# Optimization experiments

Measured on AMD Instinct MI355X. Metric: run time of the kernel, lower is better.

The kernel has to match this reference:

```python
import jax, jax.numpy as jnp
import numpy as np

B, C, H, W = 4, 512, 64, 64
RED = 8
D = max(1, C // RED)  # inter_channels = 64
BN_EPS = 1e-5


def conv1x1(x, w, b):
    # x: [B,Cin,H,W], w: [Cout,Cin], b: [Cout]
    return jnp.einsum('oc,bchw->bohw', w, x) + b[None, :, None, None]


def setup_inputs() -> dict:
    key = jax.random.key(0)
    ks = jax.random.split(key, 12)
    s = 0.02
    return {
        'x': jax.random.normal(ks[0], (B, C, H, W), jnp.float32),
        'theta_w': jax.random.normal(ks[1], (D, C), jnp.float32) * s,
        'theta_b': jax.random.normal(ks[2], (D,), jnp.float32) * s,
        'phi_w': jax.random.normal(ks[3], (D, C), jnp.float32) * s,
        'phi_b': jax.random.normal(ks[4], (D,), jnp.float32) * s,
        'g_w': jax.random.normal(ks[5], (D, C), jnp.float32) * s,
        'g_b': jax.random.normal(ks[6], (D,), jnp.float32) * s,
        'out_w': jax.random.normal(ks[7], (C, D), jnp.float32) * s,
        'out_b': jax.random.normal(ks[8], (C,), jnp.float32) * s,
        'bn_gamma': jnp.ones((C,), jnp.float32),
        'bn_beta': jnp.zeros((C,), jnp.float32),
        'scale': jax.random.normal(ks[9], (1,), jnp.float32) * 0.1,
    }


def reference(x, theta_w, theta_b, phi_w, phi_b, g_w, g_b,
              out_w, out_b, bn_gamma, bn_beta, scale):
    b, c, h, w = x.shape
    n = h * w
    theta = conv1x1(x, theta_w, theta_b).reshape(b, D, n)  # [B,D,N]
    phi = conv1x1(x, phi_w, phi_b).reshape(b, D, n)        # [B,D,N]
    g = conv1x1(x, g_w, g_b).reshape(b, D, n)              # [B,D,N]
    # attention[b,i,j] = sum_d theta[b,d,i] * phi[b,d,j] (unscaled)
    attn = jax.nn.softmax(jnp.einsum('bdi,bdj->bij', theta, phi), axis=-1)
    # y[b,d,i] = sum_j g[b,d,j] * attn[b,i,j]
    y = jnp.einsum('bdj,bij->bdi', g, attn).reshape(b, D, h, w)
    y = conv1x1(y, out_w, out_b)  # [B,C,H,W]
    # BatchNorm2d, training-mode batch statistics over (B,H,W)
    mean = jnp.mean(y, axis=(0, 2, 3), keepdims=True)
    var = jnp.var(y, axis=(0, 2, 3), keepdims=True)
    y = (y - mean) * jax.lax.rsqrt(var + BN_EPS)
    y = y * bn_gamma[None, :, None, None] + bn_beta[None, :, None, None]
    return x + scale.reshape(()) * y
```

## Files before the change

### kernel.cpp

```cpp
#include <hip/hip_runtime.h>
#include <hip/hip_bf16.h>
#include <math.h>

#define NPIX 4096
#define CIN  512
#define DD   64
#define BB   4
#define NCHUNK 8

using f32x4  = __attribute__((ext_vector_type(4))) float;
using bf16x8 = __attribute__((ext_vector_type(8))) short;
using u16x4  = __attribute__((ext_vector_type(4))) unsigned short;

__device__ __forceinline__ unsigned short f2bf(float f){
    union { __hip_bfloat16 h; unsigned short u; } v;
    v.h = __float2bfloat16(f);
    return v.u;
}

__device__ __forceinline__ unsigned pk2(float a, float b){
    union { __hip_bfloat162 h; unsigned u; } v;
    v.h = __float22bfloat162_rn(make_float2(a, b));
    return v.u;
}

__device__ __forceinline__ bf16x8 cvt8(float4 a, float4 b){
    union { unsigned u[4]; bf16x8 v; } r;
    r.u[0] = pk2(a.x, a.y); r.u[1] = pk2(a.z, a.w);
    r.u[2] = pk2(b.x, b.y); r.u[3] = pk2(b.z, b.w);
    return r.v;
}

__global__ __launch_bounds__(256) void k0_xt(
    const float* __restrict__ x, unsigned short* __restrict__ xT)
{
    const int n0 = blockIdx.x * 64;
    const int c0 = blockIdx.y * 64;
    const int b  = blockIdx.z;
    const int tid = threadIdx.x;
    __shared__ __align__(16) unsigned short T[64*72];

    {
        const int kr = tid >> 2, ns = (tid & 3) * 16;
        const float* xp = x + ((size_t)b*CIN + c0 + kr)*NPIX + n0 + ns;
        float4 a0 = *reinterpret_cast<const float4*>(xp);
        float4 a1 = *reinterpret_cast<const float4*>(xp + 4);
        float4 a2 = *reinterpret_cast<const float4*>(xp + 8);
        float4 a3 = *reinterpret_cast<const float4*>(xp + 12);
        *reinterpret_cast<bf16x8*>(&T[kr*72 + ns])     = cvt8(a0, a1);
        *reinterpret_cast<bf16x8*>(&T[kr*72 + ns + 8]) = cvt8(a2, a3);
    }
    __syncthreads();
    {
        const int nr = tid >> 2, ks = (tid & 3) * 16;
        unsigned short v[16];
        #pragma unroll
        for (int i=0;i<16;++i) v[i] = T[(ks+i)*72 + nr];
        unsigned short* dst = xT + ((size_t)b*NPIX + n0 + nr)*CIN + c0 + ks;
        *reinterpret_cast<bf16x8*>(dst)     = *reinterpret_cast<bf16x8*>(&v[0]);
        *reinterpret_cast<bf16x8*>(dst + 8) = *reinterpret_cast<bf16x8*>(&v[8]);
    }
}

__global__ __launch_bounds__(256, 4) void k1_qkv(
    const unsigned short* __restrict__ xT,
    const float* __restrict__ tw, const float* __restrict__ tbv,
    const float* __restrict__ pw, const float* __restrict__ pbv,
    const float* __restrict__ gw, const float* __restrict__ gbv,
    unsigned short* __restrict__ thetaT, unsigned short* __restrict__ phiT,
    unsigned short* __restrict__ g_dn)
{
    const int n0 = blockIdx.x * 64;
    const int kt = blockIdx.y;
    const int b  = blockIdx.z;
    const int tid = threadIdx.x;
    const float* W  = (kt==0) ? tw  : (kt==1) ? pw  : gw;
    const float* Bv = (kt==0) ? tbv : (kt==1) ? pbv : gbv;

    const int wq   = tid >> 6;
    const int lane = tid & 63;
    const int lr   = lane & 15;
    const int lg   = lane >> 4;

    __shared__ __align__(16) short Wt[64*72];
    __shared__ __align__(16) short Xt[64*72];

    f32x4 acc[4];
    #pragma unroll
    for (int jt=0;jt<4;++jt) acc[jt] = (f32x4){0.f,0.f,0.f,0.f};

    const int srow = tid >> 2;
    const int skq  = (tid & 3) * 16;

    for (int k0 = 0; k0 < CIN; k0 += 64) {
        __syncthreads();
        {
            const float* wp = W + (size_t)srow*CIN + k0 + skq;
            float4 w0 = *reinterpret_cast<const float4*>(wp);
            float4 w1 = *reinterpret_cast<const float4*>(wp + 4);
            float4 w2 = *reinterpret_cast<const float4*>(wp + 8);
            float4 w3 = *reinterpret_cast<const float4*>(wp + 12);
            *reinterpret_cast<bf16x8*>(&Wt[srow*72 + skq])     = cvt8(w0, w1);
            *reinterpret_cast<bf16x8*>(&Wt[srow*72 + skq + 8]) = cvt8(w2, w3);
            const unsigned short* xp = xT + ((size_t)b*NPIX + n0 + srow)*CIN + k0 + skq;
            *reinterpret_cast<bf16x8*>(&Xt[srow*72 + skq]) =
                *reinterpret_cast<const bf16x8*>(xp);
            *reinterpret_cast<bf16x8*>(&Xt[srow*72 + skq + 8]) =
                *reinterpret_cast<const bf16x8*>(xp + 8);
        }
        __syncthreads();

        __builtin_amdgcn_s_setprio(1);
        #pragma unroll
        for (int dc=0;dc<2;++dc){
            bf16x8 af = *reinterpret_cast<const bf16x8*>(&Wt[(wq*16+lr)*72 + dc*32 + lg*8]);
            #pragma unroll
            for (int jt=0;jt<4;++jt){
                bf16x8 bf = *reinterpret_cast<const bf16x8*>(&Xt[(jt*16+lr)*72 + dc*32 + lg*8]);
                acc[jt] = __builtin_amdgcn_mfma_f32_16x16x32_bf16(af, bf, acc[jt], 0,0,0);
            }
        }
        __builtin_amdgcn_s_setprio(0);
    }

    const int mb = wq*16 + lg*4;
    float bv[4];
    #pragma unroll
    for (int r=0;r<4;++r) bv[r] = Bv[mb+r];

    if (kt < 2){
        unsigned short* dst = (kt==0) ? thetaT : phiT;
        #pragma unroll
        for (int jt=0;jt<4;++jt){
            union { unsigned u[2]; u16x4 v; } o;
            o.u[0] = pk2(acc[jt][0]+bv[0], acc[jt][1]+bv[1]);
            o.u[1] = pk2(acc[jt][2]+bv[2], acc[jt][3]+bv[3]);
            *reinterpret_cast<u16x4*>(&dst[((size_t)b*NPIX + n0 + jt*16+lr)*DD + mb]) = o.v;
        }
    } else {
        #pragma unroll
        for (int jt=0;jt<4;++jt)
            #pragma unroll
            for (int r=0;r<4;++r)
                g_dn[((size_t)b*DD + mb+r)*NPIX + n0 + jt*16+lr] = f2bf(acc[jt][r]+bv[r]);
    }
}

__global__ __launch_bounds__(256, 4) void k2_attn(
    const unsigned short* __restrict__ thetaT,
    const unsigned short* __restrict__ phiT,
    const unsigned short* __restrict__ g_dn,
    float* __restrict__ pY, float* __restrict__ pL)
{
    const int i0 = blockIdx.x * 64;
    const int ch = blockIdx.y;
    const int b  = blockIdx.z;
    const int tid  = threadIdx.x;
    const int wq   = tid >> 6;
    const int lane = tid & 63;
    const int lr   = lane & 15;
    const int lg   = lane >> 4;

    __shared__ __align__(16) short Kt[64*72];
    __shared__ __align__(16) short Gt[64*72];
    __shared__ __align__(16) short Pb[4*16*72];
    short* Pw = &Pb[wq*16*72];

    bf16x8 qf[2];
    {
        const unsigned short* qp = thetaT + ((size_t)b*NPIX + i0 + wq*16 + lr)*DD + lg*8;
        qf[0] = *reinterpret_cast<const bf16x8*>(qp);
        qf[1] = *reinterpret_cast<const bf16x8*>(qp + 32);
    }
    const bf16x8 onesf = { (short)0x3F80,(short)0x3F80,(short)0x3F80,(short)0x3F80,
                           (short)0x3F80,(short)0x3F80,(short)0x3F80,(short)0x3F80 };

    f32x4 yacc[4], lacc;
    #pragma unroll
    for (int dt=0;dt<4;++dt) yacc[dt] = (f32x4){0.f,0.f,0.f,0.f};
    lacc = (f32x4){0.f,0.f,0.f,0.f};

    const unsigned short* phb = phiT + (size_t)b*NPIX*DD;
    const unsigned short* gb  = g_dn + (size_t)b*DD*NPIX;

    const int jbeg = ch * (NPIX / NCHUNK);
    const int jend = jbeg + (NPIX / NCHUNK);

    const int srow = tid >> 3;
    const int scb  = (tid & 7) * 8;

    for (int j0 = jbeg; j0 < jend; j0 += 64) {
        __syncthreads();
        *reinterpret_cast<float4*>(&Kt[srow*72 + scb]) =
            *reinterpret_cast<const float4*>(&phb[(size_t)(j0+srow)*DD + scb]);
        *reinterpret_cast<float4*>(&Kt[(srow+32)*72 + scb]) =
            *reinterpret_cast<const float4*>(&phb[(size_t)(j0+srow+32)*DD + scb]);
        *reinterpret_cast<float4*>(&Gt[srow*72 + scb]) =
            *reinterpret_cast<const float4*>(&gb[(size_t)srow*NPIX + j0 + scb]);
        *reinterpret_cast<float4*>(&Gt[(srow+32)*72 + scb]) =
            *reinterpret_cast<const float4*>(&gb[(size_t)(srow+32)*NPIX + j0 + scb]);
        __syncthreads();

        f32x4 s[4];
        #pragma unroll
        for (int jt=0;jt<4;++jt) s[jt] = (f32x4){0.f,0.f,0.f,0.f};
        __builtin_amdgcn_s_setprio(1);
        #pragma unroll
        for (int dc=0;dc<2;++dc){
            #pragma unroll
            for (int jt=0;jt<4;++jt){
                bf16x8 bf = *reinterpret_cast<const bf16x8*>(&Kt[(jt*16+lr)*72 + dc*32 + lg*8]);
                s[jt] = __builtin_amdgcn_mfma_f32_16x16x32_bf16(qf[dc], bf, s[jt], 0,0,0);
            }
        }
        __builtin_amdgcn_s_setprio(0);

        #pragma unroll
        for (int jt=0;jt<4;++jt)
            #pragma unroll
            for (int r=0;r<4;++r){
                float p = __expf(fminf(s[jt][r], 60.f));
                Pw[(lg*4+r)*72 + jt*16 + lr] = (short)f2bf(p);
            }

        __builtin_amdgcn_s_setprio(1);
        #pragma unroll
        for (int jc=0;jc<2;++jc){
            bf16x8 af = *reinterpret_cast<const bf16x8*>(&Pw[lr*72 + jc*32 + lg*8]);
            #pragma unroll
            for (int dt=0;dt<4;++dt){
                bf16x8 gf = *reinterpret_cast<const bf16x8*>(&Gt[(dt*16+lr)*72 + jc*32 + lg*8]);
                yacc[dt] = __builtin_amdgcn_mfma_f32_16x16x32_bf16(af, gf, yacc[dt], 0,0,0);
            }
            lacc = __builtin_amdgcn_mfma_f32_16x16x32_bf16(af, onesf, lacc, 0,0,0);
        }
        __builtin_amdgcn_s_setprio(0);
    }

    float* py = pY + (((size_t)b*NCHUNK + ch)*NPIX + i0 + wq*16)*DD;
    #pragma unroll
    for (int r=0;r<4;++r){
        #pragma unroll
        for (int dt=0;dt<4;++dt)
            py[(size_t)(lg*4+r)*DD + dt*16 + lr] = yacc[dt][r];
    }
    if (lr == 0){
        const size_t base = ((size_t)b*NCHUNK + ch)*NPIX + i0 + wq*16;
        #pragma unroll
        for (int r=0;r<4;++r)
            pL[base + lg*4+r] = lacc[r];
    }
}

__global__ __launch_bounds__(256) void k2c_combine(
    const float* __restrict__ pY, const float* __restrict__ pL,
    unsigned short* __restrict__ yTb)
{
    const int gid = blockIdx.x*256 + threadIdx.x;
    const int d  = gid & (DD-1);
    const int qn = gid >> 6;
    const int b  = qn >> 12;
    const int i  = qn & (NPIX-1);

    float lsum = 0.f, y = 0.f;
    #pragma unroll
    for (int c=0;c<NCHUNK;++c){
        lsum += pL[((size_t)b*NCHUNK + c)*NPIX + i];
        y    += pY[(((size_t)b*NCHUNK + c)*NPIX + i)*DD + d];
    }
    yTb[(size_t)qn*DD + d] = f2bf(y / lsum);
}

__global__ __launch_bounds__(256) void k3_out(
    const unsigned short* __restrict__ yTb, const float* __restrict__ ow,
    const float* __restrict__ ob, float* __restrict__ y2,
    float* __restrict__ psum, float* __restrict__ qsum)
{
    const int n0 = blockIdx.x * 64;
    const int c0 = blockIdx.y * 64;
    const int b  = blockIdx.z;
    const int tid = threadIdx.x;
    const int wq   = tid >> 6;
    const int lane = tid & 63;
    const int lr   = lane & 15;
    const int lg   = lane >> 4;

    __shared__ __align__(16) short Ot[64*72];
    __shared__ __align__(16) short Yt[64*72];

    {
        const int srow = tid >> 2, skq = (tid & 3) * 16;
        const float* wp = ow + (size_t)(c0+srow)*DD + skq;
        float4 w0 = *reinterpret_cast<const float4*>(wp);
        float4 w1 = *reinterpret_cast<const float4*>(wp + 4);
        float4 w2 = *reinterpret_cast<const float4*>(wp + 8);
        float4 w3 = *reinterpret_cast<const float4*>(wp + 12);
        *reinterpret_cast<bf16x8*>(&Ot[srow*72 + skq])     = cvt8(w0, w1);
        *reinterpret_cast<bf16x8*>(&Ot[srow*72 + skq + 8]) = cvt8(w2, w3);
        const unsigned short* yp = yTb + ((size_t)b*NPIX + n0 + srow)*DD + skq;
        *reinterpret_cast<bf16x8*>(&Yt[srow*72 + skq]) =
            *reinterpret_cast<const bf16x8*>(yp);
        *reinterpret_cast<bf16x8*>(&Yt[srow*72 + skq + 8]) =
            *reinterpret_cast<const bf16x8*>(yp + 8);
    }
    __syncthreads();

    f32x4 acc[4];
    #pragma unroll
    for (int jt=0;jt<4;++jt) acc[jt] = (f32x4){0.f,0.f,0.f,0.f};
    #pragma unroll
    for (int dc=0;dc<2;++dc){
        bf16x8 af = *reinterpret_cast<const bf16x8*>(&Ot[(wq*16+lr)*72 + dc*32 + lg*8]);
        #pragma unroll
        for (int jt=0;jt<4;++jt){
            bf16x8 bf = *reinterpret_cast<const bf16x8*>(&Yt[(jt*16+lr)*72 + dc*32 + lg*8]);
            acc[jt] = __builtin_amdgcn_mfma_f32_16x16x32_bf16(af, bf, acc[jt], 0,0,0);
        }
    }

    const int cb = c0 + wq*16 + lg*4;
    float bv[4];
    #pragma unroll
    for (int r=0;r<4;++r) bv[r] = ob[cb+r];

    float sr[4] = {0,0,0,0}, qr[4] = {0,0,0,0};
    #pragma unroll
    for (int jt=0;jt<4;++jt)
        #pragma unroll
        for (int r=0;r<4;++r){
            float v = acc[jt][r] + bv[r];
            y2[((size_t)b*CIN + cb+r)*NPIX + n0 + jt*16+lr] = v;
            sr[r] += v; qr[r] += v*v;
        }
    #pragma unroll
    for (int off=1; off<16; off<<=1)
        #pragma unroll
        for (int r=0;r<4;++r){
            sr[r] += __shfl_xor(sr[r], off);
            qr[r] += __shfl_xor(qr[r], off);
        }
    if (lr == 0){
        const int slot = b*64 + blockIdx.x;
        #pragma unroll
        for (int r=0;r<4;++r){
            psum[(size_t)(cb+r)*256 + slot] = sr[r];
            qsum[(size_t)(cb+r)*256 + slot] = qr[r];
        }
    }
}

__global__ __launch_bounds__(256) void k3b_stats(
    const float* __restrict__ psum, const float* __restrict__ qsum,
    float* __restrict__ meanA, float* __restrict__ invA)
{
    const int c = blockIdx.x;
    const int tid = threadIdx.x;
    float s = psum[(size_t)c*256 + tid];
    float q = qsum[(size_t)c*256 + tid];
    __shared__ float rs[256], rq[256];
    rs[tid]=s; rq[tid]=q; __syncthreads();
    for (int off=128; off; off>>=1){
        if (tid<off){ rs[tid]+=rs[tid+off]; rq[tid]+=rq[tid+off]; }
        __syncthreads();
    }
    if (tid==0){
        const float n = (float)(BB*NPIX);
        float mm = rs[0] / n;
        float v = rq[0] / n - mm*mm;
        meanA[c]=mm; invA[c]=rsqrtf(v + 1e-5f);
    }
}

__global__ __launch_bounds__(256) void k4_final(
    const float* __restrict__ x,
    const float* __restrict__ meanA, const float* __restrict__ invA,
    const float* __restrict__ gamma, const float* __restrict__ beta,
    const float* __restrict__ scale, float* out )
{
    const float sc = scale[0];
    const int total4 = BB*CIN*NPIX/4;
    for (int i4 = blockIdx.x*blockDim.x + threadIdx.x; i4 < total4;
         i4 += gridDim.x*blockDim.x){
        int c = (i4 >> 10) & (CIN-1);
        float4 xv = reinterpret_cast<const float4*>(x)[i4];
        float4 yv = reinterpret_cast<float4*>(out)[i4];
        float mm = meanA[c], iv = invA[c], g = gamma[c], bt = beta[c];
        float4 o;
        o.x = xv.x + sc*(g*(yv.x-mm)*iv + bt);
        o.y = xv.y + sc*(g*(yv.y-mm)*iv + bt);
        o.z = xv.z + sc*(g*(yv.z-mm)*iv + bt);
        o.w = xv.w + sc*(g*(yv.w-mm)*iv + bt);
        reinterpret_cast<float4*>(out)[i4] = o;
    }
}

extern "C" void kernel_launch(void* const* d_in, const int* in_sizes, int n_in,
                              void* d_out, int out_size, void* d_ws, size_t ws_size,
                              hipStream_t stream)
{
    const float* x     = (const float*)d_in[0];
    const float* tw    = (const float*)d_in[1];
    const float* tbv   = (const float*)d_in[2];
    const float* pw    = (const float*)d_in[3];
    const float* pbv   = (const float*)d_in[4];
    const float* gw    = (const float*)d_in[5];
    const float* gbv   = (const float*)d_in[6];
    const float* ow    = (const float*)d_in[7];
    const float* ob    = (const float*)d_in[8];
    const float* gamma = (const float*)d_in[9];
    const float* beta  = (const float*)d_in[10];
    const float* scale = (const float*)d_in[11];
    float* out = (float*)d_out;

    char* wsb = (char*)d_ws;
    unsigned short* thetaT = (unsigned short*)(wsb);
    unsigned short* phiT   = (unsigned short*)(wsb + 2097152);
    unsigned short* g_dn   = (unsigned short*)(wsb + 4194304);
    unsigned short* yTb    = (unsigned short*)(wsb + 6291456);
    float*          pL     = (float*)(wsb + 8388608);
    float*          psum   = (float*)(wsb + 8912896);
    float*          qsum   = (float*)(wsb + 9437184);
    float*          meanA  = (float*)(wsb + 9961472);
    float*          invA   = (float*)(wsb + 9963520);

    unsigned short* xT = (unsigned short*)d_out;
    float* pY = out;
    float* y2 = out;

    k0_xt  <<<dim3(64,8,4), 256, 0, stream>>>(x, xT);
    k1_qkv <<<dim3(64,3,4), 256, 0, stream>>>(xT, tw, tbv, pw, pbv, gw, gbv,
                                              thetaT, phiT, g_dn);
    k2_attn<<<dim3(64,NCHUNK,4), 256, 0, stream>>>(thetaT, phiT, g_dn, pY, pL);
    k2c_combine<<<4096, 256, 0, stream>>>(pY, pL, yTb);
    k3_out <<<dim3(64,8,4), 256, 0, stream>>>(yTb, ow, ob, y2, psum, qsum);
    k3b_stats<<<512, 256, 0, stream>>>(psum, qsum, meanA, invA);
    k4_final<<<2048, 256, 0, stream>>>(x, meanA, invA, gamma, beta, scale, out);
}
```

Measured before the change: 102.2 us.

## Double query rows per attention block, fold log2e into theta, store partials as bf16

Each attention wave now handles two 16-row query tiles, so every K/G tile staged in LDS feeds twice the MFMA work, and the grid in x is halved. The log2(e) factor is folded into the theta weights and bias so the softmax exponent uses exp2f directly. Partial y outputs are written as bf16 instead of fp32, and the combine kernel reads them two at a time, which halves that intermediate traffic. The cost is higher register pressure under launch_bounds(256,4), fewer blocks in the grid, and some extra rounding error in the partial sums.

```diff
diff --git a/kernel.cpp b/kernel.cpp
--- a/kernel.cpp
+++ b/kernel.cpp
@@ -16,6 +16,10 @@
     union { __hip_bfloat16 h; unsigned short u; } v;
     v.h = __float2bfloat16(f);
     return v.u;
+}
+
+__device__ __forceinline__ float bf2f(unsigned short u){
+    union { unsigned u; float f; } v; v.u = ((unsigned)u) << 16; return v.f;
 }
 
 __device__ __forceinline__ unsigned pk2(float a, float b){
@@ -76,6 +80,7 @@
     const int tid = threadIdx.x;
     const float* W  = (kt==0) ? tw  : (kt==1) ? pw  : gw;
     const float* Bv = (kt==0) ? tbv : (kt==1) ? pbv : gbv;
+    const float wsc = (kt==0) ? 1.4426950408889634f : 1.0f;
 
     const int wq   = tid >> 6;
     const int lane = tid & 63;
@@ -100,6 +105,10 @@
             float4 w1 = *reinterpret_cast<const float4*>(wp + 4);
             float4 w2 = *reinterpret_cast<const float4*>(wp + 8);
             float4 w3 = *reinterpret_cast<const float4*>(wp + 12);
+            w0.x*=wsc; w0.y*=wsc; w0.z*=wsc; w0.w*=wsc;
+            w1.x*=wsc; w1.y*=wsc; w1.z*=wsc; w1.w*=wsc;
+            w2.x*=wsc; w2.y*=wsc; w2.z*=wsc; w2.w*=wsc;
+            w3.x*=wsc; w3.y*=wsc; w3.z*=wsc; w3.w*=wsc;
             *reinterpret_cast<bf16x8*>(&Wt[srow*72 + skq])     = cvt8(w0, w1);
             *reinterpret_cast<bf16x8*>(&Wt[srow*72 + skq + 8]) = cvt8(w2, w3);
             const unsigned short* xp = xT + ((size_t)b*NPIX + n0 + srow)*CIN + k0 + skq;
@@ -126,7 +135,7 @@
     const int mb = wq*16 + lg*4;
     float bv[4];
     #pragma unroll
-    for (int r=0;r<4;++r) bv[r] = Bv[mb+r];
+    for (int r=0;r<4;++r) bv[r] = Bv[mb+r] * wsc;
 
     if (kt < 2){
         unsigned short* dst = (kt==0) ? thetaT : phiT;
@@ -150,9 +159,9 @@
     const unsigned short* __restrict__ thetaT,
     const unsigned short* __restrict__ phiT,
     const unsigned short* __restrict__ g_dn,
-    float* __restrict__ pY, float* __restrict__ pL)
-{
-    const int i0 = blockIdx.x * 64;
+    unsigned short* __restrict__ pY, float* __restrict__ pL)
+{
+    const int i0 = blockIdx.x * 128;
     const int ch = blockIdx.y;
     const int b  = blockIdx.z;
     const int tid  = threadIdx.x;
@@ -163,22 +172,29 @@
 
     __shared__ __align__(16) short Kt[64*72];
     __shared__ __align__(16) short Gt[64*72];
-    __shared__ __align__(16) short Pb[4*16*72];
-    short* Pw = &Pb[wq*16*72];
-
-    bf16x8 qf[2];
+    __shared__ __align__(16) short Pb[4*32*72];
+    short* Pw = &Pb[wq*32*72];
+
+    bf16x8 qf0[2], qf1[2];
     {
-        const unsigned short* qp = thetaT + ((size_t)b*NPIX + i0 + wq*16 + lr)*DD + lg*8;
-        qf[0] = *reinterpret_cast<const bf16x8*>(qp);
-        qf[1] = *reinterpret_cast<const bf16x8*>(qp + 32);
+        const unsigned short* qp0 = thetaT + ((size_t)b*NPIX + i0 + wq*16 + lr)*DD + lg*8;
+        qf0[0] = *reinterpret_cast<const bf16x8*>(qp0);
+        qf0[1] = *reinterpret_cast<const bf16x8*>(qp0 + 32);
+        const unsigned short* qp1 = qp0 + (size_t)64*DD;
+        qf1[0] = *reinterpret_cast<const bf16x8*>(qp1);
+        qf1[1] = *reinterpret_cast<const bf16x8*>(qp1 + 32);
     }
     const bf16x8 onesf = { (short)0x3F80,(short)0x3F80,(short)0x3F80,(short)0x3F80,
                            (short)0x3F80,(short)0x3F80,(short)0x3F80,(short)0x3F80 };
 
-    f32x4 yacc[4], lacc;
-    #pragma unroll
-    for (int dt=0;dt<4;++dt) yacc[dt] = (f32x4){0.f,0.f,0.f,0.f};
-    lacc = (f32x4){0.f,0.f,0.f,0.f};
+    f32x4 yacc0[4], yacc1[4], lacc0, lacc1;
+    #pragma unroll
+    for (int dt=0;dt<4;++dt){
+        yacc0[dt] = (f32x4){0.f,0.f,0.f,0.f};
+        yacc1[dt] = (f32x4){0.f,0.f,0.f,0.f};
+    }
+    lacc0 = (f32x4){0.f,0.f,0.f,0.f};
+    lacc1 = (f32x4){0.f,0.f,0.f,0.f};
 
     const unsigned short* phb = phiT + (size_t)b*NPIX*DD;
     const unsigned short* gb  = g_dn + (size_t)b*DD*NPIX;
@@ -201,16 +217,20 @@
             *reinterpret_cast<const float4*>(&gb[(size_t)(srow+32)*NPIX + j0 + scb]);
         __syncthreads();
 
-        f32x4 s[4];
-        #pragma unroll
-        for (int jt=0;jt<4;++jt) s[jt] = (f32x4){0.f,0.f,0.f,0.f};
+        f32x4 s0[4], s1[4];
+        #pragma unroll
+        for (int jt=0;jt<4;++jt){
+            s0[jt] = (f32x4){0.f,0.f,0.f,0.f};
+            s1[jt] = (f32x4){0.f,0.f,0.f,0.f};
+        }
         __builtin_amdgcn_s_setprio(1);
         #pragma unroll
         for (int dc=0;dc<2;++dc){
             #pragma unroll
             for (int jt=0;jt<4;++jt){
                 bf16x8 bf = *reinterpret_cast<const bf16x8*>(&Kt[(jt*16+lr)*72 + dc*32 + lg*8]);
-                s[jt] = __builtin_amdgcn_mfma_f32_16x16x32_bf16(qf[dc], bf, s[jt], 0,0,0);
+                s0[jt] = __builtin_amdgcn_mfma_f32_16x16x32_bf16(qf0[dc], bf, s0[jt], 0,0,0);
+                s1[jt] = __builtin_amdgcn_mfma_f32_16x16x32_bf16(qf1[dc], bf, s1[jt], 0,0,0);
             }
         }
         __builtin_amdgcn_s_setprio(0);
@@ -219,56 +239,68 @@
         for (int jt=0;jt<4;++jt)
             #pragma unroll
             for (int r=0;r<4;++r){
-                float p = __expf(fminf(s[jt][r], 60.f));
-                Pw[(lg*4+r)*72 + jt*16 + lr] = (short)f2bf(p);
+                Pw[(lg*4+r)*72      + jt*16 + lr] = (short)f2bf(exp2f(fminf(s0[jt][r], 86.f)));
+                Pw[(16+lg*4+r)*72   + jt*16 + lr] = (short)f2bf(exp2f(fminf(s1[jt][r], 86.f)));
             }
 
         __builtin_amdgcn_s_setprio(1);
         #pragma unroll
         for (int jc=0;jc<2;++jc){
-            bf16x8 af = *reinterpret_cast<const bf16x8*>(&Pw[lr*72 + jc*32 + lg*8]);
+            bf16x8 af0 = *reinterpret_cast<const bf16x8*>(&Pw[lr*72      + jc*32 + lg*8]);
+            bf16x8 af1 = *reinterpret_cast<const bf16x8*>(&Pw[(16+lr)*72 + jc*32 + lg*8]);
             #pragma unroll
             for (int dt=0;dt<4;++dt){
                 bf16x8 gf = *reinterpret_cast<const bf16x8*>(&Gt[(dt*16+lr)*72 + jc*32 + lg*8]);
-                yacc[dt] = __builtin_amdgcn_mfma_f32_16x16x32_bf16(af, gf, yacc[dt], 0,0,0);
-            }
-            lacc = __builtin_amdgcn_mfma_f32_16x16x32_bf16(af, onesf, lacc, 0,0,0);
+                yacc0[dt] = __builtin_amdgcn_mfma_f32_16x16x32_bf16(af0, gf, yacc0[dt], 0,0,0);
+                yacc1[dt] = __builtin_amdgcn_mfma_f32_16x16x32_bf16(af1, gf, yacc1[dt], 0,0,0);
+            }
+            lacc0 = __builtin_amdgcn_mfma_f32_16x16x32_bf16(af0, onesf, lacc0, 0,0,0);
+            lacc1 = __builtin_amdgcn_mfma_f32_16x16x32_bf16(af1, onesf, lacc1, 0,0,0);
         }
         __builtin_amdgcn_s_setprio(0);
     }
 
-    float* py = pY + (((size_t)b*NCHUNK + ch)*NPIX + i0 + wq*16)*DD;
-    #pragma unroll
-    for (int r=0;r<4;++r){
-        #pragma unroll
-        for (int dt=0;dt<4;++dt)
-            py[(size_t)(lg*4+r)*DD + dt*16 + lr] = yacc[dt][r];
-    }
-    if (lr == 0){
-        const size_t base = ((size_t)b*NCHUNK + ch)*NPIX + i0 + wq*16;
+    {
+        unsigned short* py0 = pY + (((size_t)b*NCHUNK + ch)*NPIX + i0 + wq*16)*DD;
+        unsigned short* py1 = py0 + (size_t)64*DD;
         #pragma unroll
         for (int r=0;r<4;++r)
-            pL[base + lg*4+r] = lacc[r];
+            #pragma unroll
+            for (int dt=0;dt<4;++dt){
+                py0[(size_t)(lg*4+r)*DD + dt*16 + lr] = f2bf(yacc0[dt][r]);
+                py1[(size_t)(lg*4+r)*DD + dt*16 + lr] = f2bf(yacc1[dt][r]);
+            }
+        if (lr == 0){
+            const size_t base = ((size_t)b*NCHUNK + ch)*NPIX + i0 + wq*16;
+            #pragma unroll
+            for (int r=0;r<4;++r){
+                pL[base + lg*4+r]      = lacc0[r];
+                pL[base + 64 + lg*4+r] = lacc1[r];
+            }
+        }
     }
 }
 
 __global__ __launch_bounds__(256) void k2c_combine(
-    const float* __restrict__ pY, const float* __restrict__ pL,
+    const unsigned short* __restrict__ pY, const float* __restrict__ pL,
     unsigned short* __restrict__ yTb)
 {
     const int gid = blockIdx.x*256 + threadIdx.x;
-    const int d  = gid & (DD-1);
-    const int qn = gid >> 6;
+    const int d2 = gid & 31;
+    const int qn = gid >> 5;
     const int b  = qn >> 12;
     const int i  = qn & (NPIX-1);
 
-    float lsum = 0.f, y = 0.f;
+    float lsum = 0.f, y0 = 0.f, y1 = 0.f;
     #pragma unroll
     for (int c=0;c<NCHUNK;++c){
         lsum += pL[((size_t)b*NCHUNK + c)*NPIX + i];
-        y    += pY[(((size_t)b*NCHUNK + c)*NPIX + i)*DD + d];
-    }
-    yTb[(size_t)qn*DD + d] = f2bf(y / lsum);
+        ushort2 v = *reinterpret_cast<const ushort2*>(
+            &pY[(((size_t)b*NCHUNK + c)*NPIX + i)*DD + d2*2]);
+        y0 += bf2f(v.x); y1 += bf2f(v.y);
+    }
+    float inv = 1.f / lsum;
+    *reinterpret_cast<unsigned*>(&yTb[(size_t)qn*DD + d2*2]) = pk2(y0*inv, y1*inv);
 }
 
 __global__ __launch_bounds__(256) void k3_out(
@@ -424,14 +456,14 @@
     float*          invA   = (float*)(wsb + 9963520);
 
     unsigned short* xT = (unsigned short*)d_out;
-    float* pY = out;
+    unsigned short* pY = (unsigned short*)d_out;
     float* y2 = out;
 
     k0_xt  <<<dim3(64,8,4), 256, 0, stream>>>(x, xT);
     k1_qkv <<<dim3(64,3,4), 256, 0, stream>>>(xT, tw, tbv, pw, pbv, gw, gbv,
                                               thetaT, phiT, g_dn);
-    k2_attn<<<dim3(64,NCHUNK,4), 256, 0, stream>>>(thetaT, phiT, g_dn, pY, pL);
-    k2c_combine<<<4096, 256, 0, stream>>>(pY, pL, yTb);
+    k2_attn<<<dim3(32,NCHUNK,4), 256, 0, stream>>>(thetaT, phiT, g_dn, pY, pL);
+    k2c_combine<<<2048, 256, 0, stream>>>(pY, pL, yTb);
     k3_out <<<dim3(64,8,4), 256, 0, stream>>>(yTb, ow, ob, y2, psum, qsum);
     k3b_stats<<<512, 256, 0, stream>>>(psum, qsum, meanA, invA);
     k4_final<<<2048, 256, 0, stream>>>(x, meanA, invA, gamma, beta, scale, out);
```

After: 96.71 us. 5.4% less time.
